# Kernel optimization log

Hardware: AMD Instinct MI355X
Metric: run time of the kernel (lower is better)

Reference implementation:

```python
import jax, jax.numpy as jnp
import numpy as np

N_EMB = 512
EMB_DIM = 64
BETA = 0.25


def setup_inputs() -> dict:
    key = jax.random.key(0)
    k1, k2 = jax.random.split(key)
    z = jax.random.normal(k1, (32, EMB_DIM, 64, 64), dtype=jnp.float32)
    # nn.Embedding weight init: uniform(-1/n_embeddings, 1/n_embeddings)
    codebook = jax.random.uniform(k2, (N_EMB, EMB_DIM), dtype=jnp.float32,
                                  minval=-1.0 / N_EMB, maxval=1.0 / N_EMB)
    return {"z": z, "codebook": codebook}


def reference(z, codebook):
    # z: [B, C, H, W] -> [B, H, W, C]
    z_nhwc = jnp.transpose(z, (0, 2, 3, 1))
    B, H, W, C = z_nhwc.shape
    zf = z_nhwc.reshape(-1, C)  # [N, C]
    # squared L2 distances to each code: ||z||^2 + ||e||^2 - 2 z.e
    dist = (jnp.sum(zf * zf, axis=1, keepdims=True)
            + jnp.sum(codebook * codebook, axis=1)
            - 2.0 * jnp.matmul(zf, codebook.T))  # [N, n_emb]
    indices = jnp.argmin(dist, axis=1)  # [N]
    # one-hot @ codebook == gather (same math, efficient form)
    z_q = codebook[indices].reshape(B, H, W, C)
    embedding_loss = jnp.mean((jax.lax.stop_gradient(z_q) - z_nhwc) ** 2)
    # straight-through estimator
    z_q_st = z_nhwc + jax.lax.stop_gradient(z_q - z_nhwc)
    z_q_out = jnp.transpose(z_q_st, (0, 3, 1, 2))  # back to [B, C, H, W]
    return (embedding_loss, z_q_out, indices)
```

## Files before the change

kernel.cpp:

```cpp
#include <hip/hip_runtime.h>


#define C_DIM   64
#define N_EMB   512
#define HW      4096
#define N_PIX   (32 * HW)
#define ZQ_OFF  1
#define IDX_OFF (1 + N_PIX * C_DIM)
#define NBLK    512

typedef _Float16 half8 __attribute__((ext_vector_type(8)));
typedef float    f32x4 __attribute__((ext_vector_type(4)));
union FragH { unsigned u[4]; half8 h8; uint4 u4; _Float16 h[8]; };

__device__ __forceinline__ unsigned umn(unsigned a, unsigned b){ return a<b?a:b; }
__device__ __forceinline__ unsigned umx(unsigned a, unsigned b){ return a>b?a:b; }

__global__ __launch_bounds__(512, 4) void vq_main(
    const float* __restrict__ z,
    const float* __restrict__ cb,
    float* __restrict__ out,
    float* __restrict__ ws)
{
    __shared__ unsigned cbh[N_EMB * 32];
    __shared__ float    esh5[N_EMB];
    __shared__ float    eshx[N_EMB];
    __shared__ float    wsum[8];

    const int t = threadIdx.x;

    {
        const float* e = cb + t * C_DIM;
        float ev[64];
        #pragma unroll
        for (int q = 0; q < 16; ++q) {
            float4 v = ((const float4*)e)[q];
            ev[4*q+0]=v.x; ev[4*q+1]=v.y; ev[4*q+2]=v.z; ev[4*q+3]=v.w;
        }
        float r[8];
        #pragma unroll
        for (int i = 0; i < 8; ++i) r[i] = __fmul_rn(ev[i], ev[i]);
        #pragma unroll
        for (int k = 8; k < 64; k += 8) {
            #pragma unroll
            for (int i = 0; i < 8; ++i)
                r[i] = __fadd_rn(r[i], __fmul_rn(ev[k+i], ev[k+i]));
        }
        float es = __fadd_rn(
            __fadd_rn(__fadd_rn(r[0],r[1]), __fadd_rn(r[2],r[3])),
            __fadd_rn(__fadd_rn(r[4],r[5]), __fadd_rn(r[6],r[7])));
        eshx[t] = es;
        esh5[t] = es + 0.5f;
        unsigned hw_[32];
        #pragma unroll
        for (int w2 = 0; w2 < 32; ++w2) {
            union { _Float16 h[2]; unsigned u; } pk;
            pk.h[0] = (_Float16)(ev[2*w2]   * 512.0f);
            pk.h[1] = (_Float16)(ev[2*w2+1] * 512.0f);
            hw_[w2] = pk.u;
        }
        const int rs = t & 7;
        #pragma unroll
        for (int g = 0; g < 8; ++g) {
            int g2 = g ^ rs;
            *(uint4*)&cbh[t*32 + g2*4] =
                make_uint4(hw_[4*g], hw_[4*g+1], hw_[4*g+2], hw_[4*g+3]);
        }
    }
    __syncthreads();

    const int l   = t & 63;
    const int wv  = t >> 6;
    const int lg  = l >> 4;
    const int li  = l & 15;
    const int bb  = blockIdx.x >> 4;
    const int g20 = (lg)     ^ (li & 7);
    const int g21 = (4 + lg) ^ (li & 7);
    const int jb  = lg * 4;
    float ls = 0.f;

    const int pxw0 = blockIdx.x * 256 + wv * 32;
    const float* zb0 = z + (size_t)bb * (C_DIM * HW) + ((pxw0      + li) & (HW-1));
    const float* zb1 = z + (size_t)bb * (C_DIM * HW) + ((pxw0 + 16 + li) & (HW-1));
    FragH bA0, bA1, bB0, bB1;
    {
        const float* c0 = zb0 + (size_t)(lg*8) * HW;
        const float* c1 = zb0 + (size_t)(32 + lg*8) * HW;
        const float* c2 = zb1 + (size_t)(lg*8) * HW;
        const float* c3 = zb1 + (size_t)(32 + lg*8) * HW;
        #pragma unroll
        for (int i = 0; i < 8; ++i) {
            bA0.h[i] = (_Float16)c0[(size_t)i*HW];
            bA1.h[i] = (_Float16)c1[(size_t)i*HW];
            bB0.h[i] = (_Float16)c2[(size_t)i*HW];
            bB1.h[i] = (_Float16)c3[(size_t)i*HW];
        }
    }

    unsigned k1A=0xFFFFFFFFu,k2A=0xFFFFFFFFu,k3A=0xFFFFFFFFu;
    unsigned k1B=0xFFFFFFFFu,k2B=0xFFFFFFFFu,k3B=0xFFFFFFFFu;
    #pragma unroll 4
    for (int T = 0; T < 32; ++T) {
        const int row = T*16 + li;
        FragH a0, a1;
        a0.u4 = *(const uint4*)&cbh[row*32 + g20*4];
        a1.u4 = *(const uint4*)&cbh[row*32 + g21*4];
        f32x4 es = *(const f32x4*)&esh5[T*16 + jb];
        f32x4 accA = {0.f,0.f,0.f,0.f}, accB = {0.f,0.f,0.f,0.f};
        accA = __builtin_amdgcn_mfma_f32_16x16x32_f16(a0.h8, bA0.h8, accA, 0,0,0);
        accA = __builtin_amdgcn_mfma_f32_16x16x32_f16(a1.h8, bA1.h8, accA, 0,0,0);
        accB = __builtin_amdgcn_mfma_f32_16x16x32_f16(a0.h8, bB0.h8, accB, 0,0,0);
        accB = __builtin_amdgcn_mfma_f32_16x16x32_f16(a1.h8, bB1.h8, accB, 0,0,0);
        const int jT = T*16 + jb;
        #pragma unroll
        for (int r2 = 0; r2 < 4; ++r2) {
            float er = (r2==0)?es[0]:(r2==1)?es[1]:(r2==2)?es[2]:es[3];
            float dA = __fmaf_rn(-0.00390625f, accA[r2], er);
            float dB = __fmaf_rn(-0.00390625f, accB[r2], er);
            unsigned keyA = (__float_as_uint(dA) & 0xFFFFFE00u) | (unsigned)(jT + r2);
            unsigned keyB = (__float_as_uint(dB) & 0xFFFFFE00u) | (unsigned)(jT + r2);
            unsigned m1,M1,m2,M2;
            m1=umn(k1A,keyA); M1=umx(k1A,keyA); k1A=m1;
            m2=umn(k2A,M1);   M2=umx(k2A,M1);   k2A=m2; k3A=umn(k3A,M2);
            m1=umn(k1B,keyB); M1=umx(k1B,keyB); k1B=m1;
            m2=umn(k2B,M1);   M2=umx(k2B,M1);   k2B=m2; k3B=umn(k3B,M2);
        }
    }

    int bj0 = 1023, bj1 = 1023;
    #pragma unroll
    for (int pt = 0; pt < 2; ++pt) {
        unsigned k1 = pt ? k1B : k1A, k2 = pt ? k2B : k2A, k3 = pt ? k3B : k3A;
        const float* zb = pt ? zb1 : zb0;
        const int px = pxw0 + pt*16 + li;

        float zr[64];
        #pragma unroll
        for (int c = 0; c < 64; ++c) zr[c] = zb[(size_t)c * HW];
        float ap;
        {
            float r[8];
            #pragma unroll
            for (int i = 0; i < 8; ++i) r[i] = __fmul_rn(zr[i], zr[i]);
            #pragma unroll
            for (int k = 8; k < 64; k += 8) {
                #pragma unroll
                for (int i = 0; i < 8; ++i)
                    r[i] = __fadd_rn(r[i], __fmul_rn(zr[k+i], zr[k+i]));
            }
            ap = __fadd_rn(
                __fadd_rn(__fadd_rn(r[0],r[1]), __fadd_rn(r[2],r[3])),
                __fadd_rn(__fadd_rn(r[4],r[5]), __fadd_rn(r[6],r[7])));
        }
        unsigned kmin = umn(k1, umn(k2, k3));
        kmin = umn(kmin, __shfl_xor(kmin, 16, 64));
        kmin = umn(kmin, __shfl_xor(kmin, 32, 64));
        const float thr = __uint_as_float(kmin & 0xFFFFFE00u) + 1.2e-4f;
        float bd = 3.0e38f; int bj = 1023;

        #define RESCORE(K) do {                                               \
            float da_ = __uint_as_float((K) & 0xFFFFFE00u);                   \
            if (da_ <= thr) {                                                 \
                int j_ = (int)((K) & 511u);                                   \
                const float* er_ = cb + (size_t)j_ * 64;                      \
                float a_ = 0.f;                                               \
                _Pragma("unroll")                                             \
                for (int c_ = 0; c_ < 64; ++c_)                               \
                    a_ = __fmaf_rn(zr[c_], er_[c_], a_);                      \
                float dd_ = __fsub_rn(__fadd_rn(ap, eshx[j_]),                \
                                      __fmul_rn(2.0f, a_));                   \
                if (dd_ < bd || (dd_ == bd && j_ < bj)) { bd = dd_; bj = j_; }\
            }                                                                 \
        } while (0)
        RESCORE(k1); RESCORE(k2); RESCORE(k3);
        #undef RESCORE

        #pragma unroll
        for (int m = 16; m <= 32; m <<= 1) {
            float od = __shfl_xor(bd, m, 64);
            int   oj = __shfl_xor(bj, m, 64);
            if (od < bd || (od == bd && oj < bj)) { bd = od; bj = oj; }
        }
        if (l < 16) {
            out[IDX_OFF + px] = (float)bj;
            ls += bd;
        }
        if (pt == 0) bj0 = bj; else bj1 = bj;
    }

    {
        const int pm = l & 31;
        const int h2 = l >> 5;
        int b0 = __shfl(bj0, pm & 15, 64);
        int b1 = __shfl(bj1, pm & 15, 64);
        const int bjw = (pm >> 4) ? b1 : b0;
        const float* eb = cb + (size_t)bjw * 64;
        float* zq = out + ZQ_OFF + (size_t)bb * (C_DIM * HW) + ((pxw0 + pm) & (HW-1));
        #pragma unroll
        for (int cc = 0; cc < 32; ++cc) {
            int c = h2 * 32 + cc;
            zq[(size_t)c * HW] = eb[c];
        }
    }

    #pragma unroll
    for (int off = 32; off; off >>= 1) ls += __shfl_down(ls, off, 64);
    if (l == 0) wsum[wv] = ls;
    __syncthreads();
    if (t == 0) {
        float s = 0.f;
        #pragma unroll
        for (int i = 0; i < 8; ++i) s += wsum[i];
        ws[blockIdx.x] = s;
    }
}

__global__ __launch_bounds__(256) void vq_loss(
    const float* __restrict__ ws, float* __restrict__ out)
{
    __shared__ float sm[4];
    float v = ws[threadIdx.x] + ws[threadIdx.x + 256];
    #pragma unroll
    for (int off = 32; off; off >>= 1) v += __shfl_down(v, off, 64);
    const int lane = threadIdx.x & 63, wid = threadIdx.x >> 6;
    if (lane == 0) sm[wid] = v;
    __syncthreads();
    if (threadIdx.x == 0)
        out[0] = ((sm[0] + sm[1]) + (sm[2] + sm[3])) * (1.0f / 8388608.0f);
}

extern "C" void kernel_launch(void* const* d_in, const int* in_sizes, int n_in,
                              void* d_out, int out_size, void* d_ws, size_t ws_size,
                              hipStream_t stream)
{
    const float* z  = (const float*)d_in[0];
    const float* cb = (const float*)d_in[1];
    float* out = (float*)d_out;
    float* ws  = (float*)d_ws;

    vq_main<<<NBLK, 512, 0, stream>>>(z, cb, out, ws);
    vq_loss<<<1, 256, 0, stream>>>(ws, out);
}
```

Baseline: 45.85 us.

## Use 1024-thread blocks with one 16-pixel tile per wave and med3 top-3

Doubles the block size to 1024 threads so each wave handles a single 16-pixel tile instead of two. This halves per-wave register state and the serial work between MFMAs. The top-3 key insertion now uses v_med3_u32 inline asm instead of separate min/max chains. The aim is more wave-level parallelism and fewer VALU ops per candidate, at the cost of fewer waves per block amortizing the codebook LDS staging. Half the threads also idle during staging.

```diff
diff --git a/kernel.cpp b/kernel.cpp
--- a/kernel.cpp
+++ b/kernel.cpp
@@ -8,15 +8,20 @@
 #define ZQ_OFF  1
 #define IDX_OFF (1 + N_PIX * C_DIM)
 #define NBLK    512
+#define TPB     1024
 
 typedef _Float16 half8 __attribute__((ext_vector_type(8)));
 typedef float    f32x4 __attribute__((ext_vector_type(4)));
 union FragH { unsigned u[4]; half8 h8; uint4 u4; _Float16 h[8]; };
 
 __device__ __forceinline__ unsigned umn(unsigned a, unsigned b){ return a<b?a:b; }
-__device__ __forceinline__ unsigned umx(unsigned a, unsigned b){ return a>b?a:b; }
-
-__global__ __launch_bounds__(512, 4) void vq_main(
+__device__ __forceinline__ unsigned med3u(unsigned a, unsigned b, unsigned c){
+    unsigned r;
+    asm("v_med3_u32 %0, %1, %2, %3" : "=v"(r) : "v"(a), "v"(b), "v"(c));
+    return r;
+}
+
+__global__ __launch_bounds__(TPB, 8) void vq_main(
     const float* __restrict__ z,
     const float* __restrict__ cb,
     float* __restrict__ out,
@@ -25,11 +30,11 @@
     __shared__ unsigned cbh[N_EMB * 32];
     __shared__ float    esh5[N_EMB];
     __shared__ float    eshx[N_EMB];
-    __shared__ float    wsum[8];
+    __shared__ float    wsum[16];
 
     const int t = threadIdx.x;
 
-    {
+    if (t < N_EMB) {
         const float* e = cb + t * C_DIM;
         float ev[64];
         #pragma unroll
@@ -79,26 +84,21 @@
     const int jb  = lg * 4;
     float ls = 0.f;
 
-    const int pxw0 = blockIdx.x * 256 + wv * 32;
-    const float* zb0 = z + (size_t)bb * (C_DIM * HW) + ((pxw0      + li) & (HW-1));
-    const float* zb1 = z + (size_t)bb * (C_DIM * HW) + ((pxw0 + 16 + li) & (HW-1));
-    FragH bA0, bA1, bB0, bB1;
+    const int pxw = blockIdx.x * 256 + wv * 16 + li;
+    const float* zb = z + (size_t)bb * (C_DIM * HW) + (pxw & (HW - 1));
+
+    FragH b0, b1;
     {
-        const float* c0 = zb0 + (size_t)(lg*8) * HW;
-        const float* c1 = zb0 + (size_t)(32 + lg*8) * HW;
-        const float* c2 = zb1 + (size_t)(lg*8) * HW;
-        const float* c3 = zb1 + (size_t)(32 + lg*8) * HW;
+        const float* c0 = zb + (size_t)(lg*8) * HW;
+        const float* c1 = zb + (size_t)(32 + lg*8) * HW;
         #pragma unroll
         for (int i = 0; i < 8; ++i) {
-            bA0.h[i] = (_Float16)c0[(size_t)i*HW];
-            bA1.h[i] = (_Float16)c1[(size_t)i*HW];
-            bB0.h[i] = (_Float16)c2[(size_t)i*HW];
-            bB1.h[i] = (_Float16)c3[(size_t)i*HW];
-        }
-    }
-
-    unsigned k1A=0xFFFFFFFFu,k2A=0xFFFFFFFFu,k3A=0xFFFFFFFFu;
-    unsigned k1B=0xFFFFFFFFu,k2B=0xFFFFFFFFu,k3B=0xFFFFFFFFu;
+            b0.h[i] = (_Float16)c0[(size_t)i*HW];
+            b1.h[i] = (_Float16)c1[(size_t)i*HW];
+        }
+    }
+
+    unsigned k1 = 0xFFFFFFFFu, k2 = 0xFFFFFFFFu, k3 = 0xFFFFFFFFu;
     #pragma unroll 4
     for (int T = 0; T < 32; ++T) {
         const int row = T*16 + li;
@@ -106,99 +106,80 @@
         a0.u4 = *(const uint4*)&cbh[row*32 + g20*4];
         a1.u4 = *(const uint4*)&cbh[row*32 + g21*4];
         f32x4 es = *(const f32x4*)&esh5[T*16 + jb];
-        f32x4 accA = {0.f,0.f,0.f,0.f}, accB = {0.f,0.f,0.f,0.f};
-        accA = __builtin_amdgcn_mfma_f32_16x16x32_f16(a0.h8, bA0.h8, accA, 0,0,0);
-        accA = __builtin_amdgcn_mfma_f32_16x16x32_f16(a1.h8, bA1.h8, accA, 0,0,0);
-        accB = __builtin_amdgcn_mfma_f32_16x16x32_f16(a0.h8, bB0.h8, accB, 0,0,0);
-        accB = __builtin_amdgcn_mfma_f32_16x16x32_f16(a1.h8, bB1.h8, accB, 0,0,0);
+        f32x4 acc = {0.f,0.f,0.f,0.f};
+        acc = __builtin_amdgcn_mfma_f32_16x16x32_f16(a0.h8, b0.h8, acc, 0,0,0);
+        acc = __builtin_amdgcn_mfma_f32_16x16x32_f16(a1.h8, b1.h8, acc, 0,0,0);
         const int jT = T*16 + jb;
         #pragma unroll
         for (int r2 = 0; r2 < 4; ++r2) {
-            float er = (r2==0)?es[0]:(r2==1)?es[1]:(r2==2)?es[2]:es[3];
-            float dA = __fmaf_rn(-0.00390625f, accA[r2], er);
-            float dB = __fmaf_rn(-0.00390625f, accB[r2], er);
-            unsigned keyA = (__float_as_uint(dA) & 0xFFFFFE00u) | (unsigned)(jT + r2);
-            unsigned keyB = (__float_as_uint(dB) & 0xFFFFFE00u) | (unsigned)(jT + r2);
-            unsigned m1,M1,m2,M2;
-            m1=umn(k1A,keyA); M1=umx(k1A,keyA); k1A=m1;
-            m2=umn(k2A,M1);   M2=umx(k2A,M1);   k2A=m2; k3A=umn(k3A,M2);
-            m1=umn(k1B,keyB); M1=umx(k1B,keyB); k1B=m1;
-            m2=umn(k2B,M1);   M2=umx(k2B,M1);   k2B=m2; k3B=umn(k3B,M2);
-        }
-    }
-
-    int bj0 = 1023, bj1 = 1023;
-    #pragma unroll
-    for (int pt = 0; pt < 2; ++pt) {
-        unsigned k1 = pt ? k1B : k1A, k2 = pt ? k2B : k2A, k3 = pt ? k3B : k3A;
-        const float* zb = pt ? zb1 : zb0;
-        const int px = pxw0 + pt*16 + li;
-
-        float zr[64];
-        #pragma unroll
-        for (int c = 0; c < 64; ++c) zr[c] = zb[(size_t)c * HW];
-        float ap;
-        {
-            float r[8];
+            float d = __fmaf_rn(-0.00390625f, acc[r2], es[r2]);
+            unsigned key = (__float_as_uint(d) & 0xFFFFFE00u) | (unsigned)(jT + r2);
+            unsigned nk3 = med3u(key, k2, k3);
+            unsigned nk2 = med3u(key, k1, k2);
+            k1 = umn(k1, key); k2 = nk2; k3 = nk3;
+        }
+    }
+
+    float zr[64];
+    #pragma unroll
+    for (int c = 0; c < 64; ++c) zr[c] = zb[(size_t)c * HW];
+    float ap;
+    {
+        float r[8];
+        #pragma unroll
+        for (int i = 0; i < 8; ++i) r[i] = __fmul_rn(zr[i], zr[i]);
+        #pragma unroll
+        for (int k = 8; k < 64; k += 8) {
             #pragma unroll
-            for (int i = 0; i < 8; ++i) r[i] = __fmul_rn(zr[i], zr[i]);
-            #pragma unroll
-            for (int k = 8; k < 64; k += 8) {
-                #pragma unroll
-                for (int i = 0; i < 8; ++i)
-                    r[i] = __fadd_rn(r[i], __fmul_rn(zr[k+i], zr[k+i]));
-            }
-            ap = __fadd_rn(
-                __fadd_rn(__fadd_rn(r[0],r[1]), __fadd_rn(r[2],r[3])),
-                __fadd_rn(__fadd_rn(r[4],r[5]), __fadd_rn(r[6],r[7])));
-        }
-        unsigned kmin = umn(k1, umn(k2, k3));
-        kmin = umn(kmin, __shfl_xor(kmin, 16, 64));
-        kmin = umn(kmin, __shfl_xor(kmin, 32, 64));
-        const float thr = __uint_as_float(kmin & 0xFFFFFE00u) + 1.2e-4f;
-        float bd = 3.0e38f; int bj = 1023;
-
-        #define RESCORE(K) do {                                               \
-            float da_ = __uint_as_float((K) & 0xFFFFFE00u);                   \
-            if (da_ <= thr) {                                                 \
-                int j_ = (int)((K) & 511u);                                   \
-                const float* er_ = cb + (size_t)j_ * 64;                      \
-                float a_ = 0.f;                                               \
-                _Pragma("unroll")                                             \
-                for (int c_ = 0; c_ < 64; ++c_)                               \
-                    a_ = __fmaf_rn(zr[c_], er_[c_], a_);                      \
-                float dd_ = __fsub_rn(__fadd_rn(ap, eshx[j_]),                \
-                                      __fmul_rn(2.0f, a_));                   \
-                if (dd_ < bd || (dd_ == bd && j_ < bj)) { bd = dd_; bj = j_; }\
-            }                                                                 \
-        } while (0)
-        RESCORE(k1); RESCORE(k2); RESCORE(k3);
-        #undef RESCORE
-
-        #pragma unroll
-        for (int m = 16; m <= 32; m <<= 1) {
-            float od = __shfl_xor(bd, m, 64);
-            int   oj = __shfl_xor(bj, m, 64);
-            if (od < bd || (od == bd && oj < bj)) { bd = od; bj = oj; }
-        }
-        if (l < 16) {
-            out[IDX_OFF + px] = (float)bj;
-            ls += bd;
-        }
-        if (pt == 0) bj0 = bj; else bj1 = bj;
+            for (int i = 0; i < 8; ++i)
+                r[i] = __fadd_rn(r[i], __fmul_rn(zr[k+i], zr[k+i]));
+        }
+        ap = __fadd_rn(
+            __fadd_rn(__fadd_rn(r[0],r[1]), __fadd_rn(r[2],r[3])),
+            __fadd_rn(__fadd_rn(r[4],r[5]), __fadd_rn(r[6],r[7])));
+    }
+
+    unsigned kmin = umn(k1, umn(k2, k3));
+    kmin = umn(kmin, __shfl_xor(kmin, 16, 64));
+    kmin = umn(kmin, __shfl_xor(kmin, 32, 64));
+    const float thr = __uint_as_float(kmin & 0xFFFFFE00u) + 1.2e-4f;
+    float bd = 3.0e38f; int bj = 1023;
+
+    #define RESCORE(K) do {                                               \
+        float da_ = __uint_as_float((K) & 0xFFFFFE00u);                   \
+        if (da_ <= thr) {                                                 \
+            int j_ = (int)((K) & 511u);                                   \
+            const float* er_ = cb + (size_t)j_ * 64;                      \
+            float a_ = 0.f;                                               \
+            _Pragma("unroll")                                             \
+            for (int c_ = 0; c_ < 64; ++c_)                               \
+                a_ = __fmaf_rn(zr[c_], er_[c_], a_);                      \
+            float dd_ = __fsub_rn(__fadd_rn(ap, eshx[j_]),                \
+                                  __fmul_rn(2.0f, a_));                   \
+            if (dd_ < bd || (dd_ == bd && j_ < bj)) { bd = dd_; bj = j_; }\
+        }                                                                 \
+    } while (0)
+    RESCORE(k1); RESCORE(k2); RESCORE(k3);
+    #undef RESCORE
+
+    #pragma unroll
+    for (int m = 16; m <= 32; m <<= 1) {
+        float od = __shfl_xor(bd, m, 64);
+        int   oj = __shfl_xor(bj, m, 64);
+        if (od < bd || (od == bd && oj < bj)) { bd = od; bj = oj; }
+    }
+    if (l < 16) {
+        out[IDX_OFF + pxw] = (float)bj;
+        ls += bd;
     }
 
     {
-        const int pm = l & 31;
-        const int h2 = l >> 5;
-        int b0 = __shfl(bj0, pm & 15, 64);
-        int b1 = __shfl(bj1, pm & 15, 64);
-        const int bjw = (pm >> 4) ? b1 : b0;
-        const float* eb = cb + (size_t)bjw * 64;
-        float* zq = out + ZQ_OFF + (size_t)bb * (C_DIM * HW) + ((pxw0 + pm) & (HW-1));
-        #pragma unroll
-        for (int cc = 0; cc < 32; ++cc) {
-            int c = h2 * 32 + cc;
+        const int cq = l >> 4;
+        const float* eb = cb + (size_t)bj * 64;
+        float* zq = out + ZQ_OFF + (size_t)bb * (C_DIM * HW) + (pxw & (HW - 1));
+        #pragma unroll
+        for (int cc = 0; cc < 16; ++cc) {
+            int c = cq * 16 + cc;
             zq[(size_t)c * HW] = eb[c];
         }
     }
@@ -210,7 +191,7 @@
     if (t == 0) {
         float s = 0.f;
         #pragma unroll
-        for (int i = 0; i < 8; ++i) s += wsum[i];
+        for (int i = 0; i < 16; ++i) s += wsum[i];
         ws[blockIdx.x] = s;
     }
 }
@@ -238,6 +219,6 @@
     float* out = (float*)d_out;
     float* ws  = (float*)d_ws;
 
-    vq_main<<<NBLK, 512, 0, stream>>>(z, cb, out, ws);
+    vq_main<<<NBLK, TPB, 0, stream>>>(z, cb, out, ws);
     vq_loss<<<1, 256, 0, stream>>>(ws, out);
 }
```

Measured after the change: 69.96 us. 1.53x slower.
